# Kernel tuning notes

Measured on AMD Instinct MI355X. Metric: run time of the kernel, lower is better.

Reference implementation:

```python
import jax, jax.numpy as jnp
import numpy as np

NUM_HEADS = 8
EPS = 1e-5


def setup_inputs() -> dict:
    key = jax.random.key(0)
    ks = jax.random.split(key, 6)
    B, C, H, W = 8, 256, 32, 32
    s = 1.0 / np.sqrt(C)  # fan-in scale for 1x1 conv weights
    return {
        "x": jax.random.normal(ks[0], (B, C, H, W), jnp.float32),
        "Wq": jax.random.normal(ks[1], (C, C), jnp.float32) * s,
        "bq": jnp.zeros((C,), jnp.float32),
        "Wk": jax.random.normal(ks[2], (C, C), jnp.float32) * s,
        "bk": jnp.zeros((C,), jnp.float32),
        "Wv": jax.random.normal(ks[3], (C, C), jnp.float32) * s,
        "bv": jnp.zeros((C,), jnp.float32),
        "Wp": jax.random.normal(ks[4], (C, C), jnp.float32) * s,
        "bp": jnp.zeros((C,), jnp.float32),
        "gamma": jnp.ones((C,), jnp.float32),
        "beta": jnp.zeros((C,), jnp.float32),
    }


def _conv1x1(x, W, b):
    # 1x1 Conv2d == channel-mixing matmul: [B,C,H,W] -> [B,C,H,W]
    return jnp.einsum('oi,bihw->bohw', W, x) + b[None, :, None, None]


def reference(x, Wq, bq, Wk, bk, Wv, bv, Wp, bp, gamma, beta):
    B, C, H, W = x.shape
    nh = NUM_HEADS
    hd = C // nh
    HW = H * W

    q = _conv1x1(x, Wq, bq).reshape(B, nh, hd, HW)
    k = _conv1x1(x, Wk, bk).reshape(B, nh, hd, HW)
    v = _conv1x1(x, Wv, bv).reshape(B, nh, hd, HW)

    scores = jnp.einsum('bhdi,bhdj->bhij', q, k) / (hd ** 0.5)  # [B,nh,HW,HW]
    attn = jax.nn.softmax(scores, axis=-1)
    out = jnp.einsum('bhij,bhdj->bhdi', attn, v).reshape(B, C, H, W)

    out = _conv1x1(out, Wp, bp) + x  # residual

    # LayerNorm over channel dim (channels-last, as in original)
    o = out.transpose(0, 2, 3, 1)  # [B,H,W,C]
    mu = jnp.mean(o, axis=-1, keepdims=True)
    var = jnp.var(o, axis=-1, keepdims=True)
    o = (o - mu) * jax.lax.rsqrt(var + EPS) * gamma + beta
    return o.transpose(0, 3, 1, 2)
```

## Files before the change

### kernel.cpp

```cpp
#include <hip/hip_runtime.h>
#include <math.h>

#define NB 8
#define NC 256
#define NHW 1024
#define NHEADS 8
#define HD 32

typedef _Float16 half_t;
typedef __attribute__((ext_vector_type(8))) _Float16 half8;
typedef __attribute__((ext_vector_type(4))) _Float16 half4v;
typedef __attribute__((ext_vector_type(2))) _Float16 half2v;
typedef __attribute__((ext_vector_type(4))) float floatx4;

__device__ __forceinline__ half2v pk2(float a, float b) {
    union {
        __fp16 __attribute__((ext_vector_type(2))) r;
        half2v h;
    } u;
    u.r = __builtin_amdgcn_cvt_pkrtz(a, b);
    return u.h;
}
__device__ __forceinline__ void st8h(half_t* p, half2v a, half2v b) {
    union { half2v h[2]; uint2 u; } t;
    t.h[0] = a; t.h[1] = b;
    *(uint2*)p = t.u;
}

__global__ __launch_bounds__(256) void wprep(
    const float* __restrict__ Wq, const float* __restrict__ Wk,
    const float* __restrict__ Wv, const float* __restrict__ Wp,
    half_t* __restrict__ Wh)
{
    int t = blockIdx.x * 256 + threadIdx.x;
    int e = t * 8;
    int m = e >> 16, off = e & 65535;
    const float* src = (m == 0) ? Wq : (m == 1) ? Wk : (m == 2) ? Wv : Wp;
    float sc = (m == 0) ? 0.17677669529663687f * 1.4426950408889634f : 1.f;
    float4 a = *(const float4*)(src + off);
    float4 b = *(const float4*)(src + off + 4);
    union { half2v h2[4]; half8 h8; } u;
    u.h2[0] = pk2(a.x * sc, a.y * sc);
    u.h2[1] = pk2(a.z * sc, a.w * sc);
    u.h2[2] = pk2(b.x * sc, b.y * sc);
    u.h2[3] = pk2(b.z * sc, b.w * sc);
    *(half8*)&Wh[e] = u.h8;
}

__global__ __launch_bounds__(512) void qkv_mfma(
    const float* __restrict__ x, const half_t* __restrict__ Wh,
    const float* __restrict__ bq, const float* __restrict__ bk, const float* __restrict__ bv,
    half_t* __restrict__ Qt, half_t* __restrict__ Kt, half_t* __restrict__ Vv)
{
    __shared__ half_t xs[64][264];

    int bz = blockIdx.z;
    int b = bz & 7, p = bz >> 3;
    const half_t* Wf    = Wh + (size_t)p * 65536;
    const float*  bias  = (p == 0) ? bq : (p == 1) ? bk : bv;

    int t = threadIdx.x;
    int s0 = blockIdx.x * 64;
    const float* xb = x + (size_t)b * NC * NHW;

    {
        int sf = t & 15, cp = t >> 4;
        int sw = (sf & 7) << 3;
        #pragma unroll
        for (int pass = 0; pass < 4; pass++) {
            int c = cp * 2 + 64 * pass;
            int cw = c ^ sw;
            float4 a  = *(const float4*)&xb[(size_t)c * NHW + s0 + sf * 4];
            float4 bb = *(const float4*)&xb[(size_t)(c + 1) * NHW + s0 + sf * 4];
            *(half2v*)&xs[sf * 4 + 0][cw] = pk2(a.x, bb.x);
            *(half2v*)&xs[sf * 4 + 1][cw] = pk2(a.y, bb.y);
            *(half2v*)&xs[sf * 4 + 2][cw] = pk2(a.z, bb.z);
            *(half2v*)&xs[sf * 4 + 3][cw] = pk2(a.w, bb.w);
        }
    }
    __syncthreads();

    int wv = t >> 6, lane = t & 63;
    int mm = lane & 15, q = lane >> 4;
    int o0 = wv * 32;

    floatx4 acc[2][4];
    #pragma unroll
    for (int mt = 0; mt < 2; mt++)
        #pragma unroll
        for (int nt = 0; nt < 4; nt++) acc[mt][nt] = (floatx4){0.f, 0.f, 0.f, 0.f};

    #pragma unroll
    for (int k0 = 0; k0 < NC; k0 += 32) {
        half8 af[2], bf[4];
        #pragma unroll
        for (int mt = 0; mt < 2; mt++)
            af[mt] = *(const half8*)&Wf[(size_t)(o0 + mt * 16 + mm) * NC + k0 + q * 8];
        #pragma unroll
        for (int nt = 0; nt < 4; nt++) {
            int row = nt * 16 + mm;
            int col = (k0 + q * 8) ^ (((row >> 2) & 7) << 3);
            bf[nt] = *(const half8*)&xs[row][col];
        }
        #pragma unroll
        for (int mt = 0; mt < 2; mt++)
            #pragma unroll
            for (int nt = 0; nt < 4; nt++)
                acc[mt][nt] = __builtin_amdgcn_mfma_f32_16x16x32_f16(af[mt], bf[nt], acc[mt][nt], 0, 0, 0);
    }

    int h  = wv;
    int bh = b * NHEADS + h;
    const float qs = 0.17677669529663687f * 1.4426950408889634f;
    float bsc = (p == 0) ? qs : 1.f;

    #pragma unroll
    for (int mt = 0; mt < 2; mt++) {
        int d0 = mt * 16 + q * 4;
        float bb[4];
        #pragma unroll
        for (int r = 0; r < 4; r++) bb[r] = bias[o0 + mt * 16 + q * 4 + r] * bsc;
        #pragma unroll
        for (int nt = 0; nt < 4; nt++) {
            int s = s0 + nt * 16 + mm;
            float v0 = acc[mt][nt][0] + bb[0], v1 = acc[mt][nt][1] + bb[1];
            float v2 = acc[mt][nt][2] + bb[2], v3 = acc[mt][nt][3] + bb[3];
            if (p < 2) {
                half_t* out = (p == 0 ? Qt : Kt) + ((size_t)bh * NHW + s) * HD + d0;
                st8h(out, pk2(v0, v1), pk2(v2, v3));
            } else {
                Vv[((size_t)bh * HD + d0 + 0) * NHW + s] = (half_t)v0;
                Vv[((size_t)bh * HD + d0 + 1) * NHW + s] = (half_t)v1;
                Vv[((size_t)bh * HD + d0 + 2) * NHW + s] = (half_t)v2;
                Vv[((size_t)bh * HD + d0 + 3) * NHW + s] = (half_t)v3;
            }
        }
    }
}

__global__ __launch_bounds__(256) void attn_mfma(
    const half_t* __restrict__ Qt, const half_t* __restrict__ Kt,
    const half_t* __restrict__ Vv, half_t* __restrict__ At)
{
    __shared__ half_t Pl[4][4][2][16][36];
    __shared__ float Oz[4][32][66];
    __shared__ float Dz[4][64];

    int wv = threadIdx.x >> 6, lane = threadIdx.x & 63;
    int mm = lane & 15, q = lane >> 4;
    int L = blockIdx.x;
    int bh = L & 63, iblk = L >> 6;
    int b = bh >> 3, h = bh & 7;
    int i0 = iblk * 64;

    const half_t* Qb = Qt + (size_t)bh * NHW * HD;
    const half_t* Kb = Kt + (size_t)bh * NHW * HD;
    const half_t* Vb = Vv + (size_t)bh * HD * NHW;

    half8 qf[4];
    #pragma unroll
    for (int qt = 0; qt < 4; qt++)
        qf[qt] = *(const half8*)&Qb[(size_t)(i0 + qt * 16 + mm) * HD + q * 8];

    const int jb = wv * 256;
    floatx4 zero = (floatx4){0.f, 0.f, 0.f, 0.f};
    floatx4 oa[4][2];
    #pragma unroll
    for (int qt = 0; qt < 4; qt++) { oa[qt][0] = zero; oa[qt][1] = zero; }
    float dd[4] = {0.f, 0.f, 0.f, 0.f};
    const _Float16 z = (_Float16)0.f;
    half8 pf[4];
    #pragma unroll
    for (int qt = 0; qt < 4; qt++) pf[qt] = (half8){z, z, z, z, z, z, z, z};

    half8 kc0 = *(const half8*)&Kb[(size_t)(jb + mm) * HD + q * 8];
    half8 kc1 = *(const half8*)&Kb[(size_t)(jb + 16 + mm) * HD + q * 8];
    half8 kn0 = *(const half8*)&Kb[(size_t)(jb + 32 + mm) * HD + q * 8];
    half8 kn1 = *(const half8*)&Kb[(size_t)(jb + 48 + mm) * HD + q * 8];
    half8 vc0 = *(const half8*)&Vb[(size_t)mm * NHW + jb + q * 8];
    half8 vc1 = *(const half8*)&Vb[(size_t)(16 + mm) * NHW + jb + q * 8];
    half8 vp0 = vc0, vp1 = vc1;

    #pragma unroll
    for (int it = 0; it < 8; it++) {
        floatx4 s[4][2];
        #pragma unroll
        for (int qt = 0; qt < 4; qt++) {
            s[qt][0] = __builtin_amdgcn_mfma_f32_16x16x32_f16(kc0, qf[qt], zero, 0, 0, 0);
            s[qt][1] = __builtin_amdgcn_mfma_f32_16x16x32_f16(kc1, qf[qt], zero, 0, 0, 0);
        }

        int jk = jb + ((it + 2) & 7) * 32;
        int jv = jb + ((it + 1) & 7) * 32;
        half8 kf0 = *(const half8*)&Kb[(size_t)(jk + mm) * HD + q * 8];
        half8 kf1 = *(const half8*)&Kb[(size_t)(jk + 16 + mm) * HD + q * 8];
        half8 vn0 = *(const half8*)&Vb[(size_t)mm * NHW + jv + q * 8];
        half8 vn1 = *(const half8*)&Vb[(size_t)(16 + mm) * NHW + jv + q * 8];

        #pragma unroll
        for (int qt = 0; qt < 4; qt++) {
            oa[qt][0] = __builtin_amdgcn_mfma_f32_16x16x32_f16(vp0, pf[qt], oa[qt][0], 0, 0, 0);
            oa[qt][1] = __builtin_amdgcn_mfma_f32_16x16x32_f16(vp1, pf[qt], oa[qt][1], 0, 0, 0);
        }

        int buf = it & 1;
        #pragma unroll
        for (int qt = 0; qt < 4; qt++) {
            float e0 = exp2f(s[qt][0][0]), e1 = exp2f(s[qt][0][1]);
            float e2 = exp2f(s[qt][0][2]), e3 = exp2f(s[qt][0][3]);
            float f0 = exp2f(s[qt][1][0]), f1 = exp2f(s[qt][1][1]);
            float f2 = exp2f(s[qt][1][2]), f3 = exp2f(s[qt][1][3]);
            dd[qt] += ((e0 + e1) + (e2 + e3)) + ((f0 + f1) + (f2 + f3));
            half_t (*PB)[36] = Pl[wv][qt][buf];
            st8h(&PB[mm][q * 4],      pk2(e0, e1), pk2(e2, e3));
            st8h(&PB[mm][16 + q * 4], pk2(f0, f1), pk2(f2, f3));
        }
        #pragma unroll
        for (int qt = 0; qt < 4; qt++) {
            union { half4v h4[2]; half8 h8; } u;
            u.h4[0] = *(half4v*)&Pl[wv][qt][buf][mm][q * 8];
            u.h4[1] = *(half4v*)&Pl[wv][qt][buf][mm][q * 8 + 4];
            pf[qt] = u.h8;
        }

        kc0 = kn0; kc1 = kn1; kn0 = kf0; kn1 = kf1;
        vp0 = vc0; vp1 = vc1; vc0 = vn0; vc1 = vn1;
    }
    #pragma unroll
    for (int qt = 0; qt < 4; qt++) {
        oa[qt][0] = __builtin_amdgcn_mfma_f32_16x16x32_f16(vp0, pf[qt], oa[qt][0], 0, 0, 0);
        oa[qt][1] = __builtin_amdgcn_mfma_f32_16x16x32_f16(vp1, pf[qt], oa[qt][1], 0, 0, 0);
    }

    #pragma unroll
    for (int qt = 0; qt < 4; qt++) {
        dd[qt] += __shfl_xor(dd[qt], 16);
        dd[qt] += __shfl_xor(dd[qt], 32);
    }

    #pragma unroll
    for (int qt = 0; qt < 4; qt++)
        #pragma unroll
        for (int r = 0; r < 4; r++) {
            Oz[wv][q * 4 + r][qt * 16 + mm]      = oa[qt][0][r];
            Oz[wv][16 + q * 4 + r][qt * 16 + mm] = oa[qt][1][r];
        }
    if (q == 0) {
        #pragma unroll
        for (int qt = 0; qt < 4; qt++) Dz[wv][qt * 16 + mm] = dd[qt];
    }
    __syncthreads();

    int t = threadIdx.x;
    int iloc = t >> 2, dg = t & 3;
    float den = (Dz[0][iloc] + Dz[1][iloc]) + (Dz[2][iloc] + Dz[3][iloc]);
    float rinv = 1.f / den;
    float v[8];
    #pragma unroll
    for (int r = 0; r < 8; r++) {
        int d = dg * 8 + r;
        v[r] = ((Oz[0][d][iloc] + Oz[1][d][iloc]) + (Oz[2][d][iloc] + Oz[3][d][iloc])) * rinv;
    }
    half_t* dst = At + ((size_t)b * NHW + i0 + iloc) * NC + h * HD + dg * 8;
    st8h(dst,     pk2(v[0], v[1]), pk2(v[2], v[3]));
    st8h(dst + 4, pk2(v[4], v[5]), pk2(v[6], v[7]));
}

__global__ __launch_bounds__(512) void projln(
    const half_t* __restrict__ At, const half_t* __restrict__ Wph,
    const float* __restrict__ bp, const float* __restrict__ x,
    const float* __restrict__ gamma, const float* __restrict__ beta,
    float* __restrict__ outp)
{
    __shared__ float tile[32][273];
    __shared__ float xs[256][33];
    __shared__ float Pz[4][64][33];
    __shared__ float ps[16][32], ps2[16][32];
    __shared__ float mu_s[32], rs_s[32];

    int t = threadIdx.x, wv = t >> 6, lane = t & 63;
    int mm = lane & 15, q = lane >> 4;
    int oh = wv & 3, kh = wv >> 2;
    int o0 = oh * 64;
    int b = blockIdx.y, s0 = blockIdx.x * 32;
    const half_t* ab = At + (size_t)b * NHW * NC;

    {
        int sL = t & 31, cb = t >> 5;
        #pragma unroll
        for (int pass = 0; pass < 16; pass++) {
            int c = pass * 16 + cb;
            xs[c][sL] = x[((size_t)b * NC + c) * NHW + s0 + sL];
        }
    }

    floatx4 acc[4][2];
    #pragma unroll
    for (int mt = 0; mt < 4; mt++)
        #pragma unroll
        for (int nt = 0; nt < 2; nt++) acc[mt][nt] = (floatx4){0.f, 0.f, 0.f, 0.f};

    int kbase = kh * 128;
    #pragma unroll
    for (int kk = 0; kk < 128; kk += 32) {
        int k0 = kbase + kk;
        half8 bf[2];
        #pragma unroll
        for (int nt = 0; nt < 2; nt++)
            bf[nt] = *(const half8*)&ab[(size_t)(s0 + nt * 16 + mm) * NC + k0 + q * 8];
        #pragma unroll
        for (int mt = 0; mt < 4; mt++) {
            half8 af = *(const half8*)&Wph[(size_t)(o0 + mt * 16 + mm) * NC + k0 + q * 8];
            #pragma unroll
            for (int nt = 0; nt < 2; nt++)
                acc[mt][nt] = __builtin_amdgcn_mfma_f32_16x16x32_f16(af, bf[nt], acc[mt][nt], 0, 0, 0);
        }
    }

    if (kh == 1) {
        #pragma unroll
        for (int mt = 0; mt < 4; mt++)
            #pragma unroll
            for (int nt = 0; nt < 2; nt++)
                #pragma unroll
                for (int r = 0; r < 4; r++)
                    Pz[oh][mt * 16 + q * 4 + r][nt * 16 + mm] = acc[mt][nt][r];
    }
    __syncthreads();
    if (kh == 0) {
        #pragma unroll
        for (int mt = 0; mt < 4; mt++) {
            #pragma unroll
            for (int nt = 0; nt < 2; nt++) {
                #pragma unroll
                for (int r = 0; r < 4; r++) {
                    int ol = mt * 16 + q * 4 + r;
                    int o = o0 + ol;
                    int sl = nt * 16 + mm;
                    tile[sl][o] = acc[mt][nt][r] + Pz[oh][ol][sl] + bp[o] + xs[o][sl];
                }
            }
        }
    }
    __syncthreads();

    int sL = t & 31, part = t >> 5;
    float sum = 0.f, sq = 0.f;
    #pragma unroll
    for (int cc = 0; cc < 16; cc++) {
        float v = tile[sL][part * 16 + cc];
        sum += v; sq += v * v;
    }
    ps[part][sL] = sum; ps2[part][sL] = sq;
    __syncthreads();
    if (t < 32) {
        float S = 0.f, S2 = 0.f;
        #pragma unroll
        for (int p2 = 0; p2 < 16; p2++) { S += ps[p2][t]; S2 += ps2[p2][t]; }
        float mu  = S * (1.f / NC);
        float var = S2 * (1.f / NC) - mu * mu;
        mu_s[t] = mu;
        rs_s[t] = rsqrtf(var + 1e-5f);
    }
    __syncthreads();
    float mu = mu_s[sL], rs = rs_s[sL];
    float* ob = outp + (size_t)b * NC * NHW;
    #pragma unroll
    for (int cc = 0; cc < 16; cc++) {
        int c = part * 16 + cc;
        ob[(size_t)c * NHW + s0 + sL] = (tile[sL][c] - mu) * rs * gamma[c] + beta[c];
    }
}

extern "C" void kernel_launch(void* const* d_in, const int* in_sizes, int n_in,
                              void* d_out, int out_size, void* d_ws, size_t ws_size,
                              hipStream_t stream)
{
    const float* x     = (const float*)d_in[0];
    const float* Wq    = (const float*)d_in[1];
    const float* bq    = (const float*)d_in[2];
    const float* Wk    = (const float*)d_in[3];
    const float* bk    = (const float*)d_in[4];
    const float* Wv    = (const float*)d_in[5];
    const float* bv    = (const float*)d_in[6];
    const float* Wp    = (const float*)d_in[7];
    const float* bp    = (const float*)d_in[8];
    const float* gamma = (const float*)d_in[9];
    const float* beta  = (const float*)d_in[10];
    float* out = (float*)d_out;

    char* w = (char*)d_ws;
    half_t* Qt = (half_t*)(w);
    half_t* Kt = (half_t*)(w + ((size_t)4  << 20));
    half_t* Vv = (half_t*)(w + ((size_t)8  << 20));
    half_t* At = (half_t*)(w + ((size_t)12 << 20));
    half_t* Wh = (half_t*)(w + ((size_t)16 << 20));

    wprep<<<dim3(128), 256, 0, stream>>>(Wq, Wk, Wv, Wp, Wh);
    qkv_mfma<<<dim3(16, 1, 24), 512, 0, stream>>>(x, Wh, bq, bk, bv, Qt, Kt, Vv);
    attn_mfma<<<dim3(1024), 256, 0, stream>>>(Qt, Kt, Vv, At);
    projln<<<dim3(32, 8), 512, 0, stream>>>(At, Wh + 3 * 65536, bp, x, gamma, beta, out);
}
```

Baseline: 128.4 us.

## Shrink attention LDS with atomic cross-wave reduction and simpler prefetch pipeline

Cuts the attention kernel's shared memory by using a single-buffered P tile and one shared output/denominator buffer that all four waves accumulate into with LDS atomicAdd, instead of per-wave buffers. The software pipeline is simplified: P·V now runs right after the softmax exp in the same iteration, and K/V prefetch depth drops from two stages to one. A launch bound of 4 blocks per CU is added to raise occupancy. In exchange it pays for LDS float atomics and an extra zero-init barrier, loses latency hiding from the deeper prefetch, and makes the summation order nondeterministic.

```diff
diff --git a/kernel.cpp b/kernel.cpp
--- a/kernel.cpp
+++ b/kernel.cpp
@@ -138,13 +138,13 @@
     }
 }
 
-__global__ __launch_bounds__(256) void attn_mfma(
+__global__ __launch_bounds__(256, 4) void attn_mfma(
     const half_t* __restrict__ Qt, const half_t* __restrict__ Kt,
     const half_t* __restrict__ Vv, half_t* __restrict__ At)
 {
-    __shared__ half_t Pl[4][4][2][16][36];
-    __shared__ float Oz[4][32][66];
-    __shared__ float Dz[4][64];
+    __shared__ half_t Pl[4][4][16][36];
+    __shared__ float Oz[32][66];
+    __shared__ float Dz[64];
 
     int wv = threadIdx.x >> 6, lane = threadIdx.x & 63;
     int mm = lane & 15, q = lane >> 4;
@@ -153,6 +153,14 @@
     int b = bh >> 3, h = bh & 7;
     int i0 = iblk * 64;
 
+    {
+        int t = threadIdx.x;
+        float* oz = &Oz[0][0];
+        for (int idx = t; idx < 32 * 66; idx += 256) oz[idx] = 0.f;
+        if (t < 64) Dz[t] = 0.f;
+    }
+    __syncthreads();
+
     const half_t* Qb = Qt + (size_t)bh * NHW * HD;
     const half_t* Kb = Kt + (size_t)bh * NHW * HD;
     const half_t* Vb = Vv + (size_t)bh * HD * NHW;
@@ -168,21 +176,20 @@
     #pragma unroll
     for (int qt = 0; qt < 4; qt++) { oa[qt][0] = zero; oa[qt][1] = zero; }
     float dd[4] = {0.f, 0.f, 0.f, 0.f};
-    const _Float16 z = (_Float16)0.f;
-    half8 pf[4];
-    #pragma unroll
-    for (int qt = 0; qt < 4; qt++) pf[qt] = (half8){z, z, z, z, z, z, z, z};
 
     half8 kc0 = *(const half8*)&Kb[(size_t)(jb + mm) * HD + q * 8];
     half8 kc1 = *(const half8*)&Kb[(size_t)(jb + 16 + mm) * HD + q * 8];
-    half8 kn0 = *(const half8*)&Kb[(size_t)(jb + 32 + mm) * HD + q * 8];
-    half8 kn1 = *(const half8*)&Kb[(size_t)(jb + 48 + mm) * HD + q * 8];
     half8 vc0 = *(const half8*)&Vb[(size_t)mm * NHW + jb + q * 8];
     half8 vc1 = *(const half8*)&Vb[(size_t)(16 + mm) * NHW + jb + q * 8];
-    half8 vp0 = vc0, vp1 = vc1;
 
     #pragma unroll
     for (int it = 0; it < 8; it++) {
+        int jn = jb + ((it + 1) & 7) * 32;
+        half8 kn0 = *(const half8*)&Kb[(size_t)(jn + mm) * HD + q * 8];
+        half8 kn1 = *(const half8*)&Kb[(size_t)(jn + 16 + mm) * HD + q * 8];
+        half8 vn0 = *(const half8*)&Vb[(size_t)mm * NHW + jn + q * 8];
+        half8 vn1 = *(const half8*)&Vb[(size_t)(16 + mm) * NHW + jn + q * 8];
+
         floatx4 s[4][2];
         #pragma unroll
         for (int qt = 0; qt < 4; qt++) {
@@ -190,20 +197,6 @@
             s[qt][1] = __builtin_amdgcn_mfma_f32_16x16x32_f16(kc1, qf[qt], zero, 0, 0, 0);
         }
 
-        int jk = jb + ((it + 2) & 7) * 32;
-        int jv = jb + ((it + 1) & 7) * 32;
-        half8 kf0 = *(const half8*)&Kb[(size_t)(jk + mm) * HD + q * 8];
-        half8 kf1 = *(const half8*)&Kb[(size_t)(jk + 16 + mm) * HD + q * 8];
-        half8 vn0 = *(const half8*)&Vb[(size_t)mm * NHW + jv + q * 8];
-        half8 vn1 = *(const half8*)&Vb[(size_t)(16 + mm) * NHW + jv + q * 8];
-
-        #pragma unroll
-        for (int qt = 0; qt < 4; qt++) {
-            oa[qt][0] = __builtin_amdgcn_mfma_f32_16x16x32_f16(vp0, pf[qt], oa[qt][0], 0, 0, 0);
-            oa[qt][1] = __builtin_amdgcn_mfma_f32_16x16x32_f16(vp1, pf[qt], oa[qt][1], 0, 0, 0);
-        }
-
-        int buf = it & 1;
         #pragma unroll
         for (int qt = 0; qt < 4; qt++) {
             float e0 = exp2f(s[qt][0][0]), e1 = exp2f(s[qt][0][1]);
@@ -211,25 +204,20 @@
             float f0 = exp2f(s[qt][1][0]), f1 = exp2f(s[qt][1][1]);
             float f2 = exp2f(s[qt][1][2]), f3 = exp2f(s[qt][1][3]);
             dd[qt] += ((e0 + e1) + (e2 + e3)) + ((f0 + f1) + (f2 + f3));
-            half_t (*PB)[36] = Pl[wv][qt][buf];
+            half_t (*PB)[36] = Pl[wv][qt];
             st8h(&PB[mm][q * 4],      pk2(e0, e1), pk2(e2, e3));
             st8h(&PB[mm][16 + q * 4], pk2(f0, f1), pk2(f2, f3));
         }
         #pragma unroll
         for (int qt = 0; qt < 4; qt++) {
             union { half4v h4[2]; half8 h8; } u;
-            u.h4[0] = *(half4v*)&Pl[wv][qt][buf][mm][q * 8];
-            u.h4[1] = *(half4v*)&Pl[wv][qt][buf][mm][q * 8 + 4];
-            pf[qt] = u.h8;
-        }
-
-        kc0 = kn0; kc1 = kn1; kn0 = kf0; kn1 = kf1;
-        vp0 = vc0; vp1 = vc1; vc0 = vn0; vc1 = vn1;
-    }
-    #pragma unroll
-    for (int qt = 0; qt < 4; qt++) {
-        oa[qt][0] = __builtin_amdgcn_mfma_f32_16x16x32_f16(vp0, pf[qt], oa[qt][0], 0, 0, 0);
-        oa[qt][1] = __builtin_amdgcn_mfma_f32_16x16x32_f16(vp1, pf[qt], oa[qt][1], 0, 0, 0);
+            u.h4[0] = *(half4v*)&Pl[wv][qt][mm][q * 8];
+            u.h4[1] = *(half4v*)&Pl[wv][qt][mm][q * 8 + 4];
+            oa[qt][0] = __builtin_amdgcn_mfma_f32_16x16x32_f16(vc0, u.h8, oa[qt][0], 0, 0, 0);
+            oa[qt][1] = __builtin_amdgcn_mfma_f32_16x16x32_f16(vc1, u.h8, oa[qt][1], 0, 0, 0);
+        }
+
+        kc0 = kn0; kc1 = kn1; vc0 = vn0; vc1 = vn1;
     }
 
     #pragma unroll
@@ -237,30 +225,25 @@
         dd[qt] += __shfl_xor(dd[qt], 16);
         dd[qt] += __shfl_xor(dd[qt], 32);
     }
-
+    if (q == 0) {
+        #pragma unroll
+        for (int qt = 0; qt < 4; qt++) atomicAdd(&Dz[qt * 16 + mm], dd[qt]);
+    }
     #pragma unroll
     for (int qt = 0; qt < 4; qt++)
         #pragma unroll
         for (int r = 0; r < 4; r++) {
-            Oz[wv][q * 4 + r][qt * 16 + mm]      = oa[qt][0][r];
-            Oz[wv][16 + q * 4 + r][qt * 16 + mm] = oa[qt][1][r];
-        }
-    if (q == 0) {
-        #pragma unroll
-        for (int qt = 0; qt < 4; qt++) Dz[wv][qt * 16 + mm] = dd[qt];
-    }
+            atomicAdd(&Oz[q * 4 + r][qt * 16 + mm],      oa[qt][0][r]);
+            atomicAdd(&Oz[16 + q * 4 + r][qt * 16 + mm], oa[qt][1][r]);
+        }
     __syncthreads();
 
     int t = threadIdx.x;
     int iloc = t >> 2, dg = t & 3;
-    float den = (Dz[0][iloc] + Dz[1][iloc]) + (Dz[2][iloc] + Dz[3][iloc]);
-    float rinv = 1.f / den;
+    float rinv = 1.f / Dz[iloc];
     float v[8];
     #pragma unroll
-    for (int r = 0; r < 8; r++) {
-        int d = dg * 8 + r;
-        v[r] = ((Oz[0][d][iloc] + Oz[1][d][iloc]) + (Oz[2][d][iloc] + Oz[3][d][iloc])) * rinv;
-    }
+    for (int r = 0; r < 8; r++) v[r] = Oz[dg * 8 + r][iloc] * rinv;
     half_t* dst = At + ((size_t)b * NHW + i0 + iloc) * NC + h * HD + dg * 8;
     st8h(dst,     pk2(v[0], v[1]), pk2(v[2], v[3]));
     st8h(dst + 4, pk2(v[4], v[5]), pk2(v[6], v[7]));
```

After: 165.2 us. 1.29x slower.
